# Performance work log

Hardware: AMD Instinct MI355X
Metric: run time of the kernel (lower is better)

## Reference

```python
import jax, jax.numpy as jnp
import numpy as np


def setup_inputs() -> dict:
    key = jax.random.key(0)
    k1, k2 = jax.random.split(key)
    L, O, N, D = 512, 512, 64, 512
    x = jax.random.normal(k1, (L, N, D), dtype=jnp.float32)
    upfold = jax.random.normal(k2, (O, N, D), dtype=jnp.float32)
    return {"x": x, "upfold": upfold}


def reference(x, upfold):
    # x: [L, N, D], upfold: [O, N, D]
    D = x.shape[-1]
    scale = 1.0 / jnp.sqrt(jnp.asarray(D, dtype=x.dtype))
    # affinities: [L, O, N]
    affinities = jnp.einsum('lnd,ond->lon', x, upfold) * scale
    # sigmoid-attention (no softmax normalization), centered at 0
    weights = jax.nn.sigmoid(affinities) - 0.5
    # features: [L, N, D]
    features = jnp.einsum('lon,ond->lnd', weights, upfold)
    return features
```

## Files before the change

### kernel.cpp

```cpp
#include <hip/hip_runtime.h>
#include <hip/hip_bf16.h>
#include <stdint.h>


typedef __attribute__((ext_vector_type(8))) short short8;
typedef __attribute__((ext_vector_type(4))) float f32x4;

__device__ __forceinline__ uint16_t f2bf(float f) {
    uint32_t u = __builtin_bit_cast(uint32_t, f);
    uint32_t r = u + 0x7FFFu + ((u >> 16) & 1u);
    return (uint16_t)(r >> 16);
}
__device__ __forceinline__ uint32_t cvt2(float a, float b) {
    return (uint32_t)f2bf(a) | ((uint32_t)f2bf(b) << 16);
}

__global__ __launch_bounds__(256) void kPrepUp(const float* __restrict__ up,
                                               uint16_t* __restrict__ ub,
                                               uint16_t* __restrict__ ut) {
    __shared__ float tile[64][65];
    int b = blockIdx.x;
    int n = b >> 6, r = b & 63;
    int o0 = (r >> 3) << 6, d0 = (r & 7) << 6;
    int tid = threadIdx.x;
    int i  = tid >> 2;
    int jq = (tid & 3) << 4;

    const float* src = up + ((size_t)(o0 + i) * 64 + n) * 512 + d0 + jq;
    float v[16];
    #pragma unroll
    for (int c = 0; c < 16; c += 4) {
        float4 q = *reinterpret_cast<const float4*>(src + c);
        v[c] = q.x; v[c+1] = q.y; v[c+2] = q.z; v[c+3] = q.w;
        tile[i][jq+c] = q.x; tile[i][jq+c+1] = q.y;
        tile[i][jq+c+2] = q.z; tile[i][jq+c+3] = q.w;
    }
    uint32_t pk[8];
    if (ub) {
        #pragma unroll
        for (int c = 0; c < 8; ++c) pk[c] = cvt2(v[2*c], v[2*c+1]);
        uint16_t* udst = ub + ((size_t)n * 512 + o0 + i) * 512 + d0 + jq;
        *reinterpret_cast<uint4*>(udst)     = *reinterpret_cast<const uint4*>(pk);
        *reinterpret_cast<uint4*>(udst + 8) = *reinterpret_cast<const uint4*>(pk + 4);
    }
    __syncthreads();
    #pragma unroll
    for (int c = 0; c < 8; ++c) pk[c] = cvt2(tile[jq + 2*c][i], tile[jq + 2*c + 1][i]);
    uint16_t* tdst = ut + ((size_t)n * 512 + d0 + i) * 512 + o0 + jq;
    *reinterpret_cast<uint4*>(tdst)     = *reinterpret_cast<const uint4*>(pk);
    *reinterpret_cast<uint4*>(tdst + 8) = *reinterpret_cast<const uint4*>(pk + 4);
}

__global__ __launch_bounds__(256) void kPrepX(const float* __restrict__ x,
                                              uint16_t* __restrict__ xb) {
    int b = blockIdx.x;
    int tid = threadIdx.x;
    int row = b * 4 + (tid >> 6);
    int l = row >> 6, n = row & 63;
    int d0 = (tid & 63) * 8;
    const float* src = x + (size_t)row * 512 + d0;
    float4 v0 = *reinterpret_cast<const float4*>(src);
    float4 v1 = *reinterpret_cast<const float4*>(src + 4);
    uint32_t pk[4] = {cvt2(v0.x, v0.y), cvt2(v0.z, v0.w),
                      cvt2(v1.x, v1.y), cvt2(v1.z, v1.w)};
    *reinterpret_cast<uint4*>(xb + ((size_t)n * 512 + l) * 512 + d0) =
        *reinterpret_cast<const uint4*>(pk);
}

template<int MODE>
__global__ __launch_bounds__(512) void kGemm256(const uint16_t* __restrict__ A,
                                                const uint16_t* __restrict__ B,
                                                void* __restrict__ outp) {
    __shared__ uint16_t As[2][16384];
    __shared__ uint16_t Bs[2][16384];
    int bid = blockIdx.x;
    int n  = (bid & 7) * 8 + (bid >> 5);
    int t  = (bid >> 3) & 3;
    int l0 = (t >> 1) << 8, c0 = (t & 1) << 8;
    int tid = threadIdx.x, lane = tid & 63, wid = tid >> 6;
    int wr = wid >> 2, wc = wid & 3;

    const char* An = (const char*)(A + (size_t)n * 262144);
    const char* Bn = (const char*)(B + (size_t)n * 262144);
    int rsub  = lane >> 3;
    int sbyte = ((lane & 7) ^ rsub) << 4;
    const char* gA = An + (size_t)(l0 + wid * 32 + rsub) * 1024 + sbyte;
    const char* gB = Bn + (size_t)(c0 + wid * 32 + rsub) * 1024 + sbyte;

    f32x4 acc[8][4];
    #pragma unroll
    for (int m = 0; m < 8; ++m)
        #pragma unroll
        for (int nf = 0; nf < 4; ++nf) acc[m][nf] = (f32x4)(0.f);

    auto STAGE = [&](int buf, int kt) {
        const char* pA = gA + kt * 128;
        const char* pB = gB + kt * 128;
        uint16_t* lA = &As[buf][wid * 2048];
        uint16_t* lB = &Bs[buf][wid * 2048];
        #pragma unroll
        for (int j = 0; j < 4; ++j) {
            __builtin_amdgcn_global_load_lds(
                (const __attribute__((address_space(1))) uint32_t*)(pA + j * 8192),
                (__attribute__((address_space(3))) uint32_t*)(lA + j * 512), 16, 0, 0);
            __builtin_amdgcn_global_load_lds(
                (const __attribute__((address_space(1))) uint32_t*)(pB + j * 8192),
                (__attribute__((address_space(3))) uint32_t*)(lB + j * 512), 16, 0, 0);
        }
    };

    STAGE(0, 0);
    asm volatile("s_waitcnt vmcnt(0)" ::: "memory");
    __builtin_amdgcn_s_barrier();

    for (int kt = 0; kt < 8; ++kt) {
        const int cur = kt & 1;
        if (kt < 7) STAGE(cur ^ 1, kt + 1);
        const uint16_t* Ac = As[cur];
        const uint16_t* Bc = Bs[cur];
        #pragma unroll
        for (int kk = 0; kk < 2; ++kk) {
            short8 a[8], bb[4];
            int kbyte = kk * 64 + ((lane >> 4) * 16);
            #pragma unroll
            for (int nf = 0; nf < 4; ++nf) {
                int row = wc * 64 + nf * 16 + (lane & 15);
                int off = row * 128 + (kbyte ^ ((row & 7) << 4));
                bb[nf] = *reinterpret_cast<const short8*>((const char*)Bc + off);
            }
            #pragma unroll
            for (int m = 0; m < 8; ++m) {
                int row = wr * 128 + m * 16 + (lane & 15);
                int off = row * 128 + (kbyte ^ ((row & 7) << 4));
                a[m] = *reinterpret_cast<const short8*>((const char*)Ac + off);
            }
            #pragma unroll
            for (int m = 0; m < 8; ++m)
                #pragma unroll
                for (int nf = 0; nf < 4; ++nf)
                    acc[m][nf] = __builtin_amdgcn_mfma_f32_16x16x32_bf16(
                        a[m], bb[nf], acc[m][nf], 0, 0, 0);
        }
        if (kt < 7) {
            asm volatile("s_waitcnt vmcnt(0)" ::: "memory");
            __builtin_amdgcn_s_barrier();
        }
    }

    if constexpr (MODE == 1) {
        uint16_t* Wn = (uint16_t*)outp + (size_t)n * 262144;
        const float scale = 0.044194173824159216f;
        #pragma unroll
        for (int m = 0; m < 8; ++m) {
            int lrow0 = l0 + wr * 128 + m * 16 + ((lane >> 4) << 2);
            #pragma unroll
            for (int nf = 0; nf < 4; ++nf) {
                int ocol = c0 + wc * 64 + nf * 16 + (lane & 15);
                #pragma unroll
                for (int r = 0; r < 4; ++r) {
                    float aff = acc[m][nf][r] * scale;
                    float w = 1.f / (1.f + __expf(-aff)) - 0.5f;
                    Wn[(size_t)(lrow0 + r) * 512 + ocol] = f2bf(w);
                }
            }
        }
    } else {
        float* On = (float*)outp;
        #pragma unroll
        for (int m = 0; m < 8; ++m) {
            int lrow0 = l0 + wr * 128 + m * 16 + ((lane >> 4) << 2);
            #pragma unroll
            for (int nf = 0; nf < 4; ++nf) {
                int dcol = c0 + wc * 64 + nf * 16 + (lane & 15);
                #pragma unroll
                for (int r = 0; r < 4; ++r)
                    On[((size_t)(lrow0 + r) * 64 + n) * 512 + dcol] = acc[m][nf][r];
            }
        }
    }
}

__global__ __launch_bounds__(256) void kGemm1f32(const float* __restrict__ x,
                                                 const float* __restrict__ up,
                                                 uint16_t* __restrict__ W) {
    __shared__ uint16_t As[128 * 64];
    __shared__ uint16_t Bs[128 * 64];
    int b   = blockIdx.x;
    int n   = b >> 4;
    int t   = b & 15;
    int l0  = (t >> 2) << 7, o0 = (t & 3) << 7;
    int tid = threadIdx.x, lane = tid & 63, wid = tid >> 6;
    int wr = wid >> 1, wc = wid & 1;

    f32x4 acc[4][4];
    #pragma unroll
    for (int m = 0; m < 4; ++m)
        #pragma unroll
        for (int nf = 0; nf < 4; ++nf) acc[m][nf] = (f32x4)(0.f);

    int srow = tid >> 1;
    int kh   = (tid & 1) * 32;
    int swz  = (srow & 7) << 4;
    const float* aSrc = x  + ((size_t)(l0 + srow) * 64 + n) * 512 + kh;
    const float* bSrc = up + ((size_t)(o0 + srow) * 64 + n) * 512 + kh;

    for (int kt = 0; kt < 8; ++kt) {
        __syncthreads();
        const float* pA = aSrc + kt * 64;
        const float* pB = bSrc + kt * 64;
        #pragma unroll
        for (int c2 = 0; c2 < 4; ++c2) {
            float4 a0 = *reinterpret_cast<const float4*>(pA + c2 * 8);
            float4 a1 = *reinterpret_cast<const float4*>(pA + c2 * 8 + 4);
            float4 b0 = *reinterpret_cast<const float4*>(pB + c2 * 8);
            float4 b1 = *reinterpret_cast<const float4*>(pB + c2 * 8 + 4);
            uint32_t pa[4] = {cvt2(a0.x,a0.y), cvt2(a0.z,a0.w), cvt2(a1.x,a1.y), cvt2(a1.z,a1.w)};
            uint32_t pb[4] = {cvt2(b0.x,b0.y), cvt2(b0.z,b0.w), cvt2(b1.x,b1.y), cvt2(b1.z,b1.w)};
            int off = srow * 128 + (((kh * 2) + c2 * 16) ^ swz);
            *reinterpret_cast<uint4*>((char*)As + off) = *reinterpret_cast<const uint4*>(pa);
            *reinterpret_cast<uint4*>((char*)Bs + off) = *reinterpret_cast<const uint4*>(pb);
        }
        __syncthreads();
        #pragma unroll
        for (int kk = 0; kk < 2; ++kk) {
            short8 a[4], bf[4];
            int kbyte = kk * 64 + ((lane >> 4) * 16);
            #pragma unroll
            for (int m = 0; m < 4; ++m) {
                int row = wr * 64 + m * 16 + (lane & 15);
                int off = row * 128 + (kbyte ^ ((row & 7) << 4));
                a[m] = *reinterpret_cast<const short8*>((char*)As + off);
            }
            #pragma unroll
            for (int nf = 0; nf < 4; ++nf) {
                int row = wc * 64 + nf * 16 + (lane & 15);
                int off = row * 128 + (kbyte ^ ((row & 7) << 4));
                bf[nf] = *reinterpret_cast<const short8*>((char*)Bs + off);
            }
            #pragma unroll
            for (int m = 0; m < 4; ++m)
                #pragma unroll
                for (int nf = 0; nf < 4; ++nf)
                    acc[m][nf] = __builtin_amdgcn_mfma_f32_16x16x32_bf16(
                        a[m], bf[nf], acc[m][nf], 0, 0, 0);
        }
    }
    const float scale = 0.044194173824159216f;
    #pragma unroll
    for (int m = 0; m < 4; ++m) {
        int lrow0 = l0 + wr * 64 + m * 16 + ((lane >> 4) << 2);
        #pragma unroll
        for (int nf = 0; nf < 4; ++nf) {
            int ocol = o0 + wc * 64 + nf * 16 + (lane & 15);
            #pragma unroll
            for (int r = 0; r < 4; ++r) {
                float aff = acc[m][nf][r] * scale;
                float w = 1.f / (1.f + __expf(-aff)) - 0.5f;
                W[((size_t)n * 512 + (lrow0 + r)) * 512 + ocol] = f2bf(w);
            }
        }
    }
}

__global__ __launch_bounds__(256) void kGemm2Mid(const uint16_t* __restrict__ W,
                                                 const uint16_t* __restrict__ ut,
                                                 float* __restrict__ out) {
    __shared__ uint16_t As[8192];
    __shared__ uint16_t Bs[8192];
    int d = blockIdx.x;
    int n  = (d & 7) * 8 + (d >> 7);
    int t  = (d >> 3) & 15;
    int l0 = (t >> 2) << 7, c0 = (t & 3) << 7;
    int tid = threadIdx.x, lane = tid & 63, wid = tid >> 6;
    int wr = wid >> 1, wc = wid & 1;

    const char* An = (const char*)(W  + (size_t)n * 262144);
    const char* Bn = (const char*)(ut + (size_t)n * 262144);
    int rsub  = lane >> 3;
    int sbyte = ((lane & 7) ^ rsub) << 4;
    const char* gA = An + (size_t)(l0 + wid * 32 + rsub) * 1024 + sbyte;
    const char* gB = Bn + (size_t)(c0 + wid * 32 + rsub) * 1024 + sbyte;
    uint16_t* lA = As + wid * 2048;
    uint16_t* lB = Bs + wid * 2048;

    f32x4 acc[4][4];
    #pragma unroll
    for (int m = 0; m < 4; ++m)
        #pragma unroll
        for (int nf = 0; nf < 4; ++nf) acc[m][nf] = (f32x4)(0.f);

    for (int kt = 0; kt < 8; ++kt) {
        if (kt) __syncthreads();
        #pragma unroll
        for (int j = 0; j < 4; ++j) {
            __builtin_amdgcn_global_load_lds(
                (const __attribute__((address_space(1))) uint32_t*)(gA + kt * 128 + j * 8192),
                (__attribute__((address_space(3))) uint32_t*)(lA + j * 512), 16, 0, 0);
            __builtin_amdgcn_global_load_lds(
                (const __attribute__((address_space(1))) uint32_t*)(gB + kt * 128 + j * 8192),
                (__attribute__((address_space(3))) uint32_t*)(lB + j * 512), 16, 0, 0);
        }
        __syncthreads();
        #pragma unroll
        for (int kk = 0; kk < 2; ++kk) {
            short8 a[4], bb[4];
            int kbyte = kk * 64 + ((lane >> 4) * 16);
            #pragma unroll
            for (int m = 0; m < 4; ++m) {
                int row = wr * 64 + m * 16 + (lane & 15);
                int off = row * 128 + (kbyte ^ ((row & 7) << 4));
                a[m] = *reinterpret_cast<const short8*>((const char*)As + off);
            }
            #pragma unroll
            for (int nf = 0; nf < 4; ++nf) {
                int row = wc * 64 + nf * 16 + (lane & 15);
                int off = row * 128 + (kbyte ^ ((row & 7) << 4));
                bb[nf] = *reinterpret_cast<const short8*>((const char*)Bs + off);
            }
            #pragma unroll
            for (int m = 0; m < 4; ++m)
                #pragma unroll
                for (int nf = 0; nf < 4; ++nf)
                    acc[m][nf] = __builtin_amdgcn_mfma_f32_16x16x32_bf16(
                        a[m], bb[nf], acc[m][nf], 0, 0, 0);
        }
    }
    #pragma unroll
    for (int m = 0; m < 4; ++m) {
        int lrow0 = l0 + wr * 64 + m * 16 + ((lane >> 4) << 2);
        #pragma unroll
        for (int nf = 0; nf < 4; ++nf) {
            int dcol = c0 + wc * 64 + nf * 16 + (lane & 15);
            #pragma unroll
            for (int r = 0; r < 4; ++r)
                out[((size_t)(lrow0 + r) * 64 + n) * 512 + dcol] = acc[m][nf][r];
        }
    }
}

__global__ __launch_bounds__(256) void kNaive(const float* __restrict__ x,
                                              const float* __restrict__ up,
                                              float* __restrict__ out) {
    __shared__ float xr[512];
    __shared__ float w[512];
    int b = blockIdx.x;
    int l = b >> 6, n = b & 63;
    int tid = threadIdx.x;
    const float* xrow = x + ((size_t)l * 64 + n) * 512;
    xr[tid] = xrow[tid];
    xr[tid + 256] = xrow[tid + 256];
    __syncthreads();
    const float scale = 0.044194173824159216f;
    #pragma unroll
    for (int oo = 0; oo < 2; ++oo) {
        int o = tid + oo * 256;
        const float* ur = up + ((size_t)o * 64 + n) * 512;
        float s = 0.f;
        for (int dd = 0; dd < 512; ++dd) s += xr[dd] * ur[dd];
        w[o] = 1.f / (1.f + __expf(-s * scale)) - 0.5f;
    }
    __syncthreads();
    #pragma unroll
    for (int dd = 0; dd < 2; ++dd) {
        int d = tid + dd * 256;
        float f = 0.f;
        for (int o = 0; o < 512; ++o)
            f += w[o] * up[((size_t)o * 64 + n) * 512 + d];
        out[((size_t)l * 64 + n) * 512 + d] = f;
    }
}

extern "C" void kernel_launch(void* const* d_in, const int* in_sizes, int n_in,
                              void* d_out, int out_size, void* d_ws, size_t ws_size,
                              hipStream_t stream) {
    const float* x  = (const float*)d_in[0];
    const float* up = (const float*)d_in[1];
    float* out = (float*)d_out;

    const size_t MB32 = (size_t)64 * 512 * 512 * 2;
    if (ws_size >= 4 * MB32) {
        uint16_t* XB = (uint16_t*)d_ws;
        uint16_t* UB = XB + 16777216;
        uint16_t* UT = UB + 16777216;
        uint16_t* W  = UT + 16777216;
        kPrepUp<<<4096, 256, 0, stream>>>(up, UB, UT);
        kPrepX <<<8192, 256, 0, stream>>>(x, XB);
        kGemm256<1><<<256, 512, 0, stream>>>(XB, UB, W);
        kGemm256<2><<<256, 512, 0, stream>>>(W, UT, out);
    } else if (ws_size >= 2 * MB32) {
        uint16_t* UT = (uint16_t*)d_ws;
        uint16_t* W  = UT + 16777216;
        kPrepUp<<<4096, 256, 0, stream>>>(up, nullptr, UT);
        kGemm1f32<<<1024, 256, 0, stream>>>(x, up, W);
        kGemm2Mid<<<1024, 256, 0, stream>>>(W, UT, out);
    } else {
        kNaive<<<512 * 64, 256, 0, stream>>>(x, up, out);
    }
}
```

Baseline: 110.1 us.

## Fuse fp32-to-bf16 conversion into first GEMM and drop X/U prep passes

Adds a first-GEMM kernel that reads fp32 x and upfold directly and converts them to bf16 in registers with the packed convert instruction before staging them into swizzled LDS. Loads for the next k-tile are issued before the MFMA loop so they overlap compute. This removes the separate kPrepX pass and the untransposed bf16 copy of upfold, along with their workspace writes and re-reads. The cost is double the global read bytes per tile (fp32) and more register pressure inside the GEMM. The second GEMM is unchanged apart from being specialized to its output mode.

Result: slower. 113.0 us (+2.6%).

```diff
diff --git a/kernel.cpp b/kernel.cpp
--- a/kernel.cpp
+++ b/kernel.cpp
@@ -13,6 +13,11 @@
 }
 __device__ __forceinline__ uint32_t cvt2(float a, float b) {
     return (uint32_t)f2bf(a) | ((uint32_t)f2bf(b) << 16);
+}
+__device__ __forceinline__ uint32_t pkbf(float lo, float hi) {
+    uint32_t r;
+    asm("v_cvt_pk_bf16_f32 %0, %1, %2" : "=v"(r) : "v"(lo), "v"(hi));
+    return r;
 }
 
 __global__ __launch_bounds__(256) void kPrepUp(const float* __restrict__ up,
@@ -51,20 +56,111 @@
     *reinterpret_cast<uint4*>(tdst + 8) = *reinterpret_cast<const uint4*>(pk + 4);
 }
 
-__global__ __launch_bounds__(256) void kPrepX(const float* __restrict__ x,
-                                              uint16_t* __restrict__ xb) {
-    int b = blockIdx.x;
-    int tid = threadIdx.x;
-    int row = b * 4 + (tid >> 6);
-    int l = row >> 6, n = row & 63;
-    int d0 = (tid & 63) * 8;
-    const float* src = x + (size_t)row * 512 + d0;
-    float4 v0 = *reinterpret_cast<const float4*>(src);
-    float4 v1 = *reinterpret_cast<const float4*>(src + 4);
-    uint32_t pk[4] = {cvt2(v0.x, v0.y), cvt2(v0.z, v0.w),
-                      cvt2(v1.x, v1.y), cvt2(v1.z, v1.w)};
-    *reinterpret_cast<uint4*>(xb + ((size_t)n * 512 + l) * 512 + d0) =
-        *reinterpret_cast<const uint4*>(pk);
+__global__ __launch_bounds__(512, 2) void kGemm1x(const float* __restrict__ x,
+                                                  const float* __restrict__ up,
+                                                  uint16_t* __restrict__ W) {
+    __shared__ uint16_t As[2][16384];
+    __shared__ uint16_t Bs[2][16384];
+    int bid = blockIdx.x;
+    int n  = (bid & 7) * 8 + (bid >> 5);
+    int t  = (bid >> 3) & 3;
+    int l0 = (t >> 1) << 8, c0 = (t & 1) << 8;
+    int tid = threadIdx.x, lane = tid & 63, wid = tid >> 6;
+    int wr = wid >> 2, wc = wid & 3;
+
+    int srow = tid >> 1;
+    int kh   = (tid & 1) * 32;
+    const float* ax = x  + ((size_t)(l0 + srow) * 64 + n) * 512 + kh;
+    const float* bx = up + ((size_t)(c0 + srow) * 64 + n) * 512 + kh;
+
+    f32x4 acc[8][4];
+    #pragma unroll
+    for (int m = 0; m < 8; ++m)
+        #pragma unroll
+        for (int nf = 0; nf < 4; ++nf) acc[m][nf] = (f32x4)(0.f);
+
+    float4 ra[8], rb[8];
+    auto LOADR = [&](int kt) {
+        #pragma unroll
+        for (int j = 0; j < 8; ++j) {
+            ra[j] = *reinterpret_cast<const float4*>(ax + kt * 64 + j * 4);
+            rb[j] = *reinterpret_cast<const float4*>(bx + kt * 64 + j * 4);
+        }
+    };
+    auto CVTW = [&](int buf) {
+        uint32_t pa[16], pb[16];
+        #pragma unroll
+        for (int j = 0; j < 8; ++j) {
+            pa[2*j]   = pkbf(ra[j].x, ra[j].y);
+            pa[2*j+1] = pkbf(ra[j].z, ra[j].w);
+            pb[2*j]   = pkbf(rb[j].x, rb[j].y);
+            pb[2*j+1] = pkbf(rb[j].z, rb[j].w);
+        }
+        int base = srow * 128;
+        #pragma unroll
+        for (int c = 0; c < 4; ++c) {
+            int off = base + ((kh * 2 + c * 16) ^ ((srow & 7) << 4));
+            *reinterpret_cast<uint4*>((char*)As[buf] + off) =
+                *reinterpret_cast<const uint4*>(pa + c * 4);
+            *reinterpret_cast<uint4*>((char*)Bs[buf] + off) =
+                *reinterpret_cast<const uint4*>(pb + c * 4);
+        }
+    };
+
+    LOADR(0);
+    CVTW(0);
+    __syncthreads();
+
+    for (int kt = 0; kt < 8; ++kt) {
+        const int cur = kt & 1;
+        if (kt < 7) LOADR(kt + 1);
+        const uint16_t* Ac = As[cur];
+        const uint16_t* Bc = Bs[cur];
+        #pragma unroll
+        for (int kk = 0; kk < 2; ++kk) {
+            short8 a[8], bb[4];
+            int kbyte = kk * 64 + ((lane >> 4) * 16);
+            #pragma unroll
+            for (int nf = 0; nf < 4; ++nf) {
+                int row = wc * 64 + nf * 16 + (lane & 15);
+                int off = row * 128 + (kbyte ^ ((row & 7) << 4));
+                bb[nf] = *reinterpret_cast<const short8*>((const char*)Bc + off);
+            }
+            #pragma unroll
+            for (int m = 0; m < 8; ++m) {
+                int row = wr * 128 + m * 16 + (lane & 15);
+                int off = row * 128 + (kbyte ^ ((row & 7) << 4));
+                a[m] = *reinterpret_cast<const short8*>((const char*)Ac + off);
+            }
+            #pragma unroll
+            for (int m = 0; m < 8; ++m)
+                #pragma unroll
+                for (int nf = 0; nf < 4; ++nf)
+                    acc[m][nf] = __builtin_amdgcn_mfma_f32_16x16x32_bf16(
+                        a[m], bb[nf], acc[m][nf], 0, 0, 0);
+        }
+        if (kt < 7) {
+            CVTW(cur ^ 1);
+            __syncthreads();
+        }
+    }
+
+    uint16_t* Wn = W + (size_t)n * 262144;
+    const float scale = 0.044194173824159216f;
+    #pragma unroll
+    for (int m = 0; m < 8; ++m) {
+        int lrow0 = l0 + wr * 128 + m * 16 + ((lane >> 4) << 2);
+        #pragma unroll
+        for (int nf = 0; nf < 4; ++nf) {
+            int ocol = c0 + wc * 64 + nf * 16 + (lane & 15);
+            #pragma unroll
+            for (int r = 0; r < 4; ++r) {
+                float aff = acc[m][nf][r] * scale;
+                float w = 1.f / (1.f + __expf(-aff)) - 0.5f;
+                Wn[(size_t)(lrow0 + r) * 512 + ocol] = f2bf(w);
+            }
+        }
+    }
 }
 
 template<int MODE>
@@ -147,35 +243,16 @@
         }
     }
 
-    if constexpr (MODE == 1) {
-        uint16_t* Wn = (uint16_t*)outp + (size_t)n * 262144;
-        const float scale = 0.044194173824159216f;
-        #pragma unroll
-        for (int m = 0; m < 8; ++m) {
-            int lrow0 = l0 + wr * 128 + m * 16 + ((lane >> 4) << 2);
-            #pragma unroll
-            for (int nf = 0; nf < 4; ++nf) {
-                int ocol = c0 + wc * 64 + nf * 16 + (lane & 15);
-                #pragma unroll
-                for (int r = 0; r < 4; ++r) {
-                    float aff = acc[m][nf][r] * scale;
-                    float w = 1.f / (1.f + __expf(-aff)) - 0.5f;
-                    Wn[(size_t)(lrow0 + r) * 512 + ocol] = f2bf(w);
-                }
-            }
-        }
-    } else {
-        float* On = (float*)outp;
-        #pragma unroll
-        for (int m = 0; m < 8; ++m) {
-            int lrow0 = l0 + wr * 128 + m * 16 + ((lane >> 4) << 2);
-            #pragma unroll
-            for (int nf = 0; nf < 4; ++nf) {
-                int dcol = c0 + wc * 64 + nf * 16 + (lane & 15);
-                #pragma unroll
-                for (int r = 0; r < 4; ++r)
-                    On[((size_t)(lrow0 + r) * 64 + n) * 512 + dcol] = acc[m][nf][r];
-            }
+    float* On = (float*)outp;
+    #pragma unroll
+    for (int m = 0; m < 8; ++m) {
+        int lrow0 = l0 + wr * 128 + m * 16 + ((lane >> 4) << 2);
+        #pragma unroll
+        for (int nf = 0; nf < 4; ++nf) {
+            int dcol = c0 + wc * 64 + nf * 16 + (lane & 15);
+            #pragma unroll
+            for (int r = 0; r < 4; ++r)
+                On[((size_t)(lrow0 + r) * 64 + n) * 512 + dcol] = acc[m][nf][r];
         }
     }
 }
@@ -378,21 +455,12 @@
     float* out = (float*)d_out;
 
     const size_t MB32 = (size_t)64 * 512 * 512 * 2;
-    if (ws_size >= 4 * MB32) {
-        uint16_t* XB = (uint16_t*)d_ws;
-        uint16_t* UB = XB + 16777216;
-        uint16_t* UT = UB + 16777216;
-        uint16_t* W  = UT + 16777216;
-        kPrepUp<<<4096, 256, 0, stream>>>(up, UB, UT);
-        kPrepX <<<8192, 256, 0, stream>>>(x, XB);
-        kGemm256<1><<<256, 512, 0, stream>>>(XB, UB, W);
-        kGemm256<2><<<256, 512, 0, stream>>>(W, UT, out);
-    } else if (ws_size >= 2 * MB32) {
+    if (ws_size >= 2 * MB32) {
         uint16_t* UT = (uint16_t*)d_ws;
         uint16_t* W  = UT + 16777216;
         kPrepUp<<<4096, 256, 0, stream>>>(up, nullptr, UT);
-        kGemm1f32<<<1024, 256, 0, stream>>>(x, up, W);
-        kGemm2Mid<<<1024, 256, 0, stream>>>(W, UT, out);
+        kGemm1x<<<256, 512, 0, stream>>>(x, up, W);
+        kGemm256<2><<<256, 512, 0, stream>>>(W, UT, out);
     } else {
         kNaive<<<512 * 64, 256, 0, stream>>>(x, up, out);
     }
```

## Deepen GEMM pipeline to four LDS stages with smaller K tiles

Applied to the files above, without the earlier changes.

Replaces the double-buffered 128-wide K tile with a four-stage ring of 64-wide K tiles, keeping three loads in flight and waiting with partial vmcnt counts instead of draining everything. It also changes the LDS swizzle to match the 64-byte row stride and adds sched_barriers to pin the ordering. The aim is to hide global-load latency better behind the MFMA work. The trade-off is twice as many barriers per K sweep, plus a fully unrolled loop that increases code size.

New measurement: 108.0 us. Within noise of the previous version (-1.9%).

```diff
diff --git a/kernel.cpp b/kernel.cpp
--- a/kernel.cpp
+++ b/kernel.cpp
@@ -68,11 +68,11 @@
 }
 
 template<int MODE>
-__global__ __launch_bounds__(512) void kGemm256(const uint16_t* __restrict__ A,
-                                                const uint16_t* __restrict__ B,
-                                                void* __restrict__ outp) {
-    __shared__ uint16_t As[2][16384];
-    __shared__ uint16_t Bs[2][16384];
+__global__ __launch_bounds__(512) void kGemmP(const uint16_t* __restrict__ A,
+                                              const uint16_t* __restrict__ B,
+                                              void* __restrict__ outp) {
+    __shared__ __align__(16) uint16_t As[4][8192];
+    __shared__ __align__(16) uint16_t Bs[4][8192];
     int bid = blockIdx.x;
     int n  = (bid & 7) * 8 + (bid >> 5);
     int t  = (bid >> 3) & 3;
@@ -82,10 +82,15 @@
 
     const char* An = (const char*)(A + (size_t)n * 262144);
     const char* Bn = (const char*)(B + (size_t)n * 262144);
-    int rsub  = lane >> 3;
-    int sbyte = ((lane & 7) ^ rsub) << 4;
-    const char* gA = An + (size_t)(l0 + wid * 32 + rsub) * 1024 + sbyte;
-    const char* gB = Bn + (size_t)(c0 + wid * 32 + rsub) * 1024 + sbyte;
+
+    int s1 = tid, s2 = tid + 512;
+    int r1 = s1 >> 2, r2 = s2 >> 2;
+    int cg1 = (s1 & 3) ^ ((r1 >> 1) & 3);
+    int cg2 = (s2 & 3) ^ ((r2 >> 1) & 3);
+    const char* gA1 = An + (size_t)(l0 + r1) * 1024 + cg1 * 16;
+    const char* gA2 = An + (size_t)(l0 + r2) * 1024 + cg2 * 16;
+    const char* gB1 = Bn + (size_t)(c0 + r1) * 1024 + cg1 * 16;
+    const char* gB2 = Bn + (size_t)(c0 + r2) * 1024 + cg2 * 16;
 
     f32x4 acc[8][4];
     #pragma unroll
@@ -94,56 +99,68 @@
         for (int nf = 0; nf < 4; ++nf) acc[m][nf] = (f32x4)(0.f);
 
     auto STAGE = [&](int buf, int kt) {
-        const char* pA = gA + kt * 128;
-        const char* pB = gB + kt * 128;
-        uint16_t* lA = &As[buf][wid * 2048];
-        uint16_t* lB = &Bs[buf][wid * 2048];
-        #pragma unroll
-        for (int j = 0; j < 4; ++j) {
-            __builtin_amdgcn_global_load_lds(
-                (const __attribute__((address_space(1))) uint32_t*)(pA + j * 8192),
-                (__attribute__((address_space(3))) uint32_t*)(lA + j * 512), 16, 0, 0);
-            __builtin_amdgcn_global_load_lds(
-                (const __attribute__((address_space(1))) uint32_t*)(pB + j * 8192),
-                (__attribute__((address_space(3))) uint32_t*)(lB + j * 512), 16, 0, 0);
-        }
+        int ko = kt * 64;
+        uint16_t* lA = &As[buf][wid * 512];
+        uint16_t* lB = &Bs[buf][wid * 512];
+        __builtin_amdgcn_global_load_lds(
+            (const __attribute__((address_space(1))) uint32_t*)(gA1 + ko),
+            (__attribute__((address_space(3))) uint32_t*)(lA), 16, 0, 0);
+        __builtin_amdgcn_global_load_lds(
+            (const __attribute__((address_space(1))) uint32_t*)(gA2 + ko),
+            (__attribute__((address_space(3))) uint32_t*)(lA + 4096), 16, 0, 0);
+        __builtin_amdgcn_global_load_lds(
+            (const __attribute__((address_space(1))) uint32_t*)(gB1 + ko),
+            (__attribute__((address_space(3))) uint32_t*)(lB), 16, 0, 0);
+        __builtin_amdgcn_global_load_lds(
+            (const __attribute__((address_space(1))) uint32_t*)(gB2 + ko),
+            (__attribute__((address_space(3))) uint32_t*)(lB + 4096), 16, 0, 0);
     };
 
     STAGE(0, 0);
-    asm volatile("s_waitcnt vmcnt(0)" ::: "memory");
+    STAGE(1, 1);
+    STAGE(2, 2);
+    asm volatile("s_waitcnt vmcnt(8)" ::: "memory");
     __builtin_amdgcn_s_barrier();
-
-    for (int kt = 0; kt < 8; ++kt) {
-        const int cur = kt & 1;
-        if (kt < 7) STAGE(cur ^ 1, kt + 1);
-        const uint16_t* Ac = As[cur];
-        const uint16_t* Bc = Bs[cur];
-        #pragma unroll
-        for (int kk = 0; kk < 2; ++kk) {
-            short8 a[8], bb[4];
-            int kbyte = kk * 64 + ((lane >> 4) * 16);
-            #pragma unroll
-            for (int nf = 0; nf < 4; ++nf) {
-                int row = wc * 64 + nf * 16 + (lane & 15);
-                int off = row * 128 + (kbyte ^ ((row & 7) << 4));
-                bb[nf] = *reinterpret_cast<const short8*>((const char*)Bc + off);
-            }
-            #pragma unroll
-            for (int m = 0; m < 8; ++m) {
-                int row = wr * 128 + m * 16 + (lane & 15);
-                int off = row * 128 + (kbyte ^ ((row & 7) << 4));
-                a[m] = *reinterpret_cast<const short8*>((const char*)Ac + off);
-            }
-            #pragma unroll
-            for (int m = 0; m < 8; ++m)
-                #pragma unroll
-                for (int nf = 0; nf < 4; ++nf)
-                    acc[m][nf] = __builtin_amdgcn_mfma_f32_16x16x32_bf16(
-                        a[m], bb[nf], acc[m][nf], 0, 0, 0);
-        }
-        if (kt < 7) {
+    __builtin_amdgcn_sched_barrier(0);
+
+    int g = lane >> 4;
+    #pragma unroll
+    for (int kt = 0; kt < 16; ++kt) {
+        const int cur = kt & 3;
+        if (kt < 13) STAGE((kt + 3) & 3, kt + 3);
+        const char* Ac = (const char*)As[cur];
+        const char* Bc = (const char*)Bs[cur];
+        short8 a[8], bb[4];
+        #pragma unroll
+        for (int nf = 0; nf < 4; ++nf) {
+            int row = wc * 64 + nf * 16 + (lane & 15);
+            int off = row * 64 + ((g ^ ((row >> 1) & 3)) << 4);
+            bb[nf] = *reinterpret_cast<const short8*>(Bc + off);
+        }
+        #pragma unroll
+        for (int m = 0; m < 8; ++m) {
+            int row = wr * 128 + m * 16 + (lane & 15);
+            int off = row * 64 + ((g ^ ((row >> 1) & 3)) << 4);
+            a[m] = *reinterpret_cast<const short8*>(Ac + off);
+        }
+        #pragma unroll
+        for (int m = 0; m < 8; ++m)
+            #pragma unroll
+            for (int nf = 0; nf < 4; ++nf)
+                acc[m][nf] = __builtin_amdgcn_mfma_f32_16x16x32_bf16(
+                    a[m], bb[nf], acc[m][nf], 0, 0, 0);
+        if (kt < 13) {
+            asm volatile("s_waitcnt vmcnt(8)" ::: "memory");
+            __builtin_amdgcn_s_barrier();
+            __builtin_amdgcn_sched_barrier(0);
+        } else if (kt == 13) {
+            asm volatile("s_waitcnt vmcnt(4)" ::: "memory");
+            __builtin_amdgcn_s_barrier();
+            __builtin_amdgcn_sched_barrier(0);
+        } else if (kt == 14) {
             asm volatile("s_waitcnt vmcnt(0)" ::: "memory");
             __builtin_amdgcn_s_barrier();
+            __builtin_amdgcn_sched_barrier(0);
         }
     }
 
@@ -385,8 +402,8 @@
         uint16_t* W  = UT + 16777216;
         kPrepUp<<<4096, 256, 0, stream>>>(up, UB, UT);
         kPrepX <<<8192, 256, 0, stream>>>(x, XB);
-        kGemm256<1><<<256, 512, 0, stream>>>(XB, UB, W);
-        kGemm256<2><<<256, 512, 0, stream>>>(W, UT, out);
+        kGemmP<1><<<256, 512, 0, stream>>>(XB, UB, W);
+        kGemmP<2><<<256, 512, 0, stream>>>(W, UT, out);
     } else if (ws_size >= 2 * MB32) {
         uint16_t* UT = (uint16_t*)d_ws;
         uint16_t* W  = UT + 16777216;
```
